# Optimization experiments

Hardware: AMD Instinct MI355X
Metric: run time of the kernel (lower is better)

## Reference

```python
import jax, jax.numpy as jnp
import numpy as np

DIM = 1024
HEADS = 16
DIM_HEAD = DIM // HEADS
SCALE = DIM_HEAD ** -0.5
LN_EPS = 1e-5


def setup_inputs() -> dict:
    key = jax.random.key(0)
    ks = jax.random.split(key, 7)
    b, n = 4, 2048
    x = jax.random.normal(ks[0], (b, n, DIM), dtype=jnp.float32)
    pos = jax.random.normal(ks[1], (b, n, DIM), dtype=jnp.float32)
    # params (torch Linear init-like scale)
    w_qkv = jax.random.normal(ks[2], (DIM, 3 * DIM), dtype=jnp.float32) * (DIM ** -0.5)
    w_out = jax.random.normal(ks[3], (DIM, DIM), dtype=jnp.float32) * (DIM ** -0.5)
    b_out = jax.random.normal(ks[4], (DIM,), dtype=jnp.float32) * 0.01
    ln_gamma = jnp.ones((DIM,), dtype=jnp.float32)
    ln_beta = jnp.zeros((DIM,), dtype=jnp.float32)
    return {"x": x, "pos": pos, "w_qkv": w_qkv, "w_out": w_out,
            "b_out": b_out, "ln_gamma": ln_gamma, "ln_beta": ln_beta}


def _layer_norm(x, gamma, beta):
    mu = jnp.mean(x, axis=-1, keepdims=True)
    var = jnp.mean(jnp.square(x - mu), axis=-1, keepdims=True)
    return (x - mu) * jax.lax.rsqrt(var + LN_EPS) * gamma + beta


def reference(x, pos, w_qkv, w_out, b_out, ln_gamma, ln_beta):
    b, n, _ = x.shape
    xn = _layer_norm(x, ln_gamma, ln_beta)
    qkv = xn @ w_qkv                                    # [b, n, 3*dim]
    q, k, v = jnp.split(qkv, 3, axis=-1)
    # [b, n, dim] -> [b, h, n, d]
    to_heads = lambda t: t.reshape(b, n, HEADS, DIM_HEAD).transpose(0, 2, 1, 3)
    q, k, v = to_heads(q), to_heads(k), to_heads(v)
    scores = jnp.einsum('bhid,bhjd->bhij', q, k) * SCALE  # [b, h, n, n]
    attn = jax.nn.softmax(scores, axis=-1)
    out = jnp.einsum('bhij,bhjd->bhid', attn, v)          # [b, h, n, d]
    out = out.transpose(0, 2, 1, 3).reshape(b, n, DIM)    # [b, n, dim]
    return (out + pos) @ w_out + b_out
```

## Files before the change

### kernel.cpp

```cpp
#include <hip/hip_runtime.h>
#include <math.h>
#include <stdint.h>

#define TOKENS 8192
#define DIM 1024
#define N3 3072
#define NSEQ 2048
#define NH 16
#define DH 64

typedef __attribute__((ext_vector_type(8))) __bf16 bf16x8;
typedef __attribute__((ext_vector_type(4))) float f32x4;
typedef __attribute__((ext_vector_type(16))) float f32x16;
typedef __attribute__((ext_vector_type(4))) short short4v;

__device__ __forceinline__ unsigned cvt2bf(float a, float b) {
    unsigned r;
    asm("v_cvt_pk_bf16_f32 %0, %1, %2" : "=v"(r) : "v"(a), "v"(b));
    return r;
}
__device__ __forceinline__ unsigned short f2bf(float f) {
    unsigned r;
    asm("v_cvt_pk_bf16_f32 %0, %1, %1" : "=v"(r) : "v"(f));
    return (unsigned short)r;
}
__device__ __forceinline__ float exp2_raw(float x) {
    float r;
    asm("v_exp_f32 %0, %1" : "=v"(r) : "v"(x));
    return r;
}
__device__ __forceinline__ float max3f(float a, float b, float c) {
    float d;
    asm("v_max3_f32 %0, %1, %2, %3" : "=v"(d) : "v"(a), "v"(b), "v"(c));
    return d;
}

__device__ __forceinline__ void glds16(const void* g, void* l) {
    __builtin_amdgcn_global_load_lds((__attribute__((address_space(1))) void*)(void*)g,
                                     (__attribute__((address_space(3))) void*)l, 16, 0, 0);
}

__global__ __launch_bounds__(256) void transpose_to_bf16(
    const float* __restrict__ in, unsigned short* __restrict__ out, int R, int C) {
    __shared__ float tile[64][65];
    int n0 = blockIdx.x * 64, k0 = blockIdx.y * 64;
    int t = threadIdx.x;
#pragma unroll
    for (int i = 0; i < 16; i++) {
        int idx = i * 256 + t;
        int r = idx >> 6, c = idx & 63;
        tile[r][c] = in[(size_t)(k0 + r) * C + n0 + c];
    }
    __syncthreads();
#pragma unroll
    for (int i = 0; i < 16; i++) {
        int idx = i * 256 + t;
        int r = idx >> 6, c = idx & 63;
        out[(size_t)(n0 + r) * R + k0 + c] = f2bf(tile[c][r]);
    }
}

__global__ __launch_bounds__(256) void ln_kernel(
    const float* __restrict__ x, const float* __restrict__ gamma,
    const float* __restrict__ beta, unsigned short* __restrict__ xn) {
    int row = blockIdx.x;
    int t = threadIdx.x;
    const float4 v = ((const float4*)(x + (size_t)row * DIM))[t];
    float s = v.x + v.y + v.z + v.w;
    float sq = v.x * v.x + v.y * v.y + v.z * v.z + v.w * v.w;
#pragma unroll
    for (int m = 1; m < 64; m <<= 1) {
        s += __shfl_xor(s, m);
        sq += __shfl_xor(sq, m);
    }
    __shared__ float ws[4], wq[4];
    int w = t >> 6, lane = t & 63;
    if (lane == 0) { ws[w] = s; wq[w] = sq; }
    __syncthreads();
    s = ws[0] + ws[1] + ws[2] + ws[3];
    sq = wq[0] + wq[1] + wq[2] + wq[3];
    float mu = s * (1.0f / DIM);
    float var = sq * (1.0f / DIM) - mu * mu;
    float rstd = rsqrtf(var + 1e-5f);
    const float4 g = ((const float4*)gamma)[t];
    const float4 bb = ((const float4*)beta)[t];
    uint2 o;
    o.x = cvt2bf((v.x - mu) * rstd * g.x + bb.x, (v.y - mu) * rstd * g.y + bb.y);
    o.y = cvt2bf((v.z - mu) * rstd * g.z + bb.z, (v.w - mu) * rstd * g.w + bb.w);
    *(uint2*)(xn + (size_t)row * DIM + t * 4) = o;
}

__device__ __forceinline__ void xcd_swizzle(int& bx, int& by) {
    int nwgx = gridDim.x;
    int nwg = nwgx * gridDim.y;
    int wg = by * nwgx + bx;
    int cpx = nwg >> 3;
    int swz = (wg & 7) * cpx + (wg >> 3);
    bx = swz % nwgx;
    by = swz / nwgx;
}

__device__ __forceinline__ void gemm_core(
    const unsigned short* __restrict__ A, const unsigned short* __restrict__ Bt, int K,
    int brow, int bcol, short* As, short* Bs, f32x4 acc[4][4]) {
    int t = threadIdx.x, w = t >> 6, lane = t & 63;
    int wr = w >> 1, wc = w & 1;
    int srow = lane >> 2, scol = (lane & 3) * 8;
    for (int k0 = 0; k0 < K; k0 += 32) {
        __syncthreads();
#pragma unroll
        for (int i = 0; i < 2; i++) {
            int c = i * 4 + w;
            glds16(A + (size_t)(brow + 16 * c + srow) * K + k0 + scol, (char*)As + c * 1024);
            glds16(Bt + (size_t)(bcol + 16 * c + srow) * K + k0 + scol, (char*)Bs + c * 1024);
        }
        __syncthreads();
        bf16x8 a[4], b[4];
#pragma unroll
        for (int i = 0; i < 4; i++) {
            a[i] = *(const bf16x8*)&As[(wr * 64 + i * 16 + (lane & 15)) * 32 + (lane >> 4) * 8];
            b[i] = *(const bf16x8*)&Bs[(wc * 64 + i * 16 + (lane & 15)) * 32 + (lane >> 4) * 8];
        }
#pragma unroll
        for (int i = 0; i < 4; i++)
#pragma unroll
            for (int j = 0; j < 4; j++)
                acc[i][j] = __builtin_amdgcn_mfma_f32_16x16x32_bf16(a[i], b[j], acc[i][j], 0, 0, 0);
    }
}

#define QSCALE_LOG2E 0.18033688011112042f

__global__ __launch_bounds__(256) void gemm_qkv(
    const unsigned short* __restrict__ A, const unsigned short* __restrict__ Bt,
    unsigned short* __restrict__ Qb, unsigned short* __restrict__ Kb,
    unsigned short* __restrict__ Vt) {
    __shared__ __align__(16) short As[128 * 32];
    __shared__ __align__(16) short Bs[128 * 32];
    int bx = blockIdx.x, by = blockIdx.y;
    xcd_swizzle(bx, by);
    int brow = by * 128, bcol = bx * 128;
    f32x4 acc[4][4] = {};
    gemm_core(A, Bt, DIM, brow, bcol, As, Bs, acc);

    int t = threadIdx.x, w = t >> 6, lane = t & 63;
    int wr = w >> 1, wc = w & 1;
    int part = bcol >> 10;
#pragma unroll
    for (int i = 0; i < 4; i++) {
#pragma unroll
        for (int j = 0; j < 4; j++) {
            int col = bcol + wc * 64 + j * 16 + (lane & 15);
            int within = col & 1023;
            int h = within >> 6, d = within & 63;
            int rowb = brow + wr * 64 + i * 16 + (lane >> 4) * 4;
            if (part == 2) {
                int b = rowb >> 11, n = rowb & 2047;
                int bh = (b << 4) + h;
                uint2 pv;
                pv.x = cvt2bf(acc[i][j][0], acc[i][j][1]);
                pv.y = cvt2bf(acc[i][j][2], acc[i][j][3]);
                *(uint2*)(Vt + ((size_t)bh * 64 + d) * 2048 + n) = pv;
            } else {
#pragma unroll
                for (int r = 0; r < 4; r++) {
                    int row = rowb + r;
                    int b = row >> 11, n = row & 2047;
                    int bh = (b << 4) + h;
                    float val = acc[i][j][r];
                    if (part == 0)
                        Qb[((size_t)bh * 2048 + n) * 64 + d] = f2bf(val * QSCALE_LOG2E);
                    else
                        Kb[((size_t)bh * 2048 + n) * 64 + d] = f2bf(val);
                }
            }
        }
    }
}

__global__ __launch_bounds__(256) void gemm_out(
    const unsigned short* __restrict__ A, const unsigned short* __restrict__ Bt,
    const float* __restrict__ bias, float* __restrict__ out) {
    __shared__ __align__(16) short As[128 * 32];
    __shared__ __align__(16) short Bs[128 * 32];
    int bx = blockIdx.x, by = blockIdx.y;
    xcd_swizzle(bx, by);
    int brow = by * 128, bcol = bx * 128;
    f32x4 acc[4][4] = {};
    gemm_core(A, Bt, DIM, brow, bcol, As, Bs, acc);

    int t = threadIdx.x, w = t >> 6, lane = t & 63;
    int wr = w >> 1, wc = w & 1;
#pragma unroll
    for (int i = 0; i < 4; i++) {
#pragma unroll
        for (int j = 0; j < 4; j++) {
            int col = bcol + wc * 64 + j * 16 + (lane & 15);
            float bv = bias[col];
#pragma unroll
            for (int r = 0; r < 4; r++) {
                int row = brow + wr * 64 + i * 16 + (lane >> 4) * 4 + r;
                out[(size_t)row * DIM + col] = acc[i][j][r] + bv;
            }
        }
    }
}

#define LOG2E_THR 11.5f

__global__ __launch_bounds__(512, 4) void attn_kernel(
    const unsigned short* __restrict__ Qb, const unsigned short* __restrict__ Kb,
    const unsigned short* __restrict__ Vt, const float* __restrict__ pos,
    unsigned short* __restrict__ att) {
    __shared__ __align__(16) char Ks[4][8192];
    __shared__ __align__(16) char Vs[4][8192];
    int t = threadIdx.x, w = t >> 6, lane = t & 63;
    int l31 = lane & 31, lhi = lane >> 5;

    int L = blockIdx.y * gridDim.x + blockIdx.x;
    int bh = (L & 7) + (((L >> 3) & 7) << 3);
    int qt = L >> 6;
    int b = bh >> 4, h = bh & 15;
    int qr = qt * 256 + w * 32 + l31;

    const unsigned short* Qh = Qb + (size_t)bh * NSEQ * DH;
    const char* Khc = (const char*)(Kb + (size_t)bh * NSEQ * DH);
    const char* Vhc = (const char*)(Vt + (size_t)bh * DH * NSEQ);

    bf16x8 qf[4];
#pragma unroll
    for (int ks = 0; ks < 4; ks++)
        qf[ks] = *(const bf16x8*)(Qh + (size_t)qr * DH + ks * 16 + lhi * 8);

    f32x16 oacc[2] = {};
    float mrun = -INFINITY, lsum = 0.f;

    int ct = w >> 2, cs = w & 3;
    const char* Ksrc = Khc + (size_t)(ct * 32 + l31) * 128 + cs * 32 + lhi * 16;
    const char* Vsrc = Vhc + (size_t)(ct * 32 + l31) * 4096 + (size_t)(cs * 16 + lhi * 8) * 2;
    auto stage = [&](char* kbuf, char* vbuf, int kv0) {
        glds16(Ksrc + (size_t)kv0 * 128, kbuf + w * 1024);
        glds16(Vsrc + (size_t)kv0 * 2, vbuf + w * 1024);
    };

    auto compute = [&](const char* kc, const char* vc) {
        f32x16 st0 = {}, st1 = {};
        __builtin_amdgcn_s_setprio(1);
#pragma unroll
        for (int ks = 0; ks < 4; ks++) {
            bf16x8 kf = *(const bf16x8*)(kc + ks * 1024 + lane * 16);
            st0 = __builtin_amdgcn_mfma_f32_32x32x16_bf16(kf, qf[ks], st0, 0, 0, 0);
        }
#pragma unroll
        for (int ks = 0; ks < 4; ks++) {
            bf16x8 kf = *(const bf16x8*)(kc + (4 + ks) * 1024 + lane * 16);
            st1 = __builtin_amdgcn_mfma_f32_32x32x16_bf16(kf, qf[ks], st1, 0, 0, 0);
        }
        __builtin_amdgcn_s_setprio(0);

        float b0 = max3f(st0[0], st0[8], st1[0]);
        float b1 = max3f(st0[1], st0[9], st1[1]);
        float b2 = max3f(st0[2], st0[10], st1[2]);
        float b3 = max3f(st0[3], st0[11], st1[3]);
        float b4 = max3f(st0[4], st0[12], st1[4]);
        float b5 = max3f(st0[5], st0[13], st1[5]);
        float b6 = max3f(st0[6], st0[14], st1[6]);
        float b7 = max3f(st0[7], st0[15], st1[7]);
        float c0 = max3f(b0, b4, st1[8]);
        float c1 = max3f(b1, b5, st1[9]);
        float c2 = max3f(b2, b6, st1[10]);
        float c3 = max3f(b3, b7, st1[11]);
        float d0 = max3f(c0, c1, st1[12]);
        float d1 = max3f(c2, c3, st1[13]);
        float pm = max3f(d0, d1, fmaxf(st1[14], st1[15]));
        {
            float pa = pm, pb = pm;
            asm("v_permlane32_swap_b32 %0, %1" : "+v"(pa), "+v"(pb));
            pm = fmaxf(pa, pb);
        }
        if (!__all(pm - mrun <= LOG2E_THR)) {
            float mnew = fmaxf(mrun, pm);
            float scale = exp2_raw(mrun - mnew);
            lsum *= scale;
            oacc[0] *= scale;
            oacc[1] *= scale;
            mrun = mnew;
        }
        {
            float s0 = 0.f, s1 = 0.f, s2 = 0.f, s3 = 0.f;
#pragma unroll
            for (int r = 0; r < 16; r += 4) {
                float e0 = exp2_raw(st0[r] - mrun);
                float e1 = exp2_raw(st0[r + 1] - mrun);
                float e2 = exp2_raw(st0[r + 2] - mrun);
                float e3 = exp2_raw(st0[r + 3] - mrun);
                st0[r] = e0; st0[r + 1] = e1; st0[r + 2] = e2; st0[r + 3] = e3;
                s0 += e0; s1 += e1; s2 += e2; s3 += e3;
            }
#pragma unroll
            for (int r = 0; r < 16; r += 4) {
                float e0 = exp2_raw(st1[r] - mrun);
                float e1 = exp2_raw(st1[r + 1] - mrun);
                float e2 = exp2_raw(st1[r + 2] - mrun);
                float e3 = exp2_raw(st1[r + 3] - mrun);
                st1[r] = e0; st1[r + 1] = e1; st1[r + 2] = e2; st1[r + 3] = e3;
                s0 += e0; s1 += e1; s2 += e2; s3 += e3;
            }
            lsum += (s0 + s1) + (s2 + s3);
        }
        bf16x8 bfr[4];
#pragma unroll
        for (int ks = 0; ks < 4; ks++) {
            const f32x16& sv = (ks < 2) ? st0 : st1;
            int rb = (ks & 1) * 8;
            unsigned pa = cvt2bf(sv[rb + 0], sv[rb + 1]);
            unsigned pc = cvt2bf(sv[rb + 2], sv[rb + 3]);
            unsigned pb = cvt2bf(sv[rb + 4], sv[rb + 5]);
            unsigned pd = cvt2bf(sv[rb + 6], sv[rb + 7]);
            asm("v_permlane32_swap_b32 %0, %1" : "+v"(pa), "+v"(pb));
            asm("v_permlane32_swap_b32 %0, %1" : "+v"(pc), "+v"(pd));
            uint4 pw = {pa, pc, pb, pd};
            bfr[ks] = *(bf16x8*)&pw;
        }
        __builtin_amdgcn_s_setprio(1);
#pragma unroll
        for (int ks = 0; ks < 4; ks++)
#pragma unroll
            for (int dt = 0; dt < 2; dt++) {
                bf16x8 vf = *(const bf16x8*)(vc + (dt * 4 + ks) * 1024 + lane * 16);
                oacc[dt] = __builtin_amdgcn_mfma_f32_32x32x16_bf16(vf, bfr[ks], oacc[dt], 0, 0, 0);
            }
        __builtin_amdgcn_s_setprio(0);
    };

    char* kA0 = Ks[0]; char* kA1 = Ks[1]; char* kB0 = Ks[2]; char* kB1 = Ks[3];
    char* vA0 = Vs[0]; char* vA1 = Vs[1]; char* vB0 = Vs[2]; char* vB1 = Vs[3];
    stage(kA0, vA0, 0);
    stage(kA1, vA1, 64);

    for (int p = 0; p < 32; p += 2) {
        asm volatile("s_waitcnt vmcnt(2)" ::: "memory");
        __builtin_amdgcn_s_barrier();
        stage(kB0, vB0, ((p + 2) & 31) << 6);
        stage(kB1, vB1, ((p + 3) & 31) << 6);
        compute(kA0, vA0);
        asm volatile("s_waitcnt vmcnt(4)" ::: "memory");
        compute(kA1, vA1);
        char* tp;
        tp = kA0; kA0 = kB0; kB0 = tp;  tp = kA1; kA1 = kB1; kB1 = tp;
        tp = vA0; vA0 = vB0; vB0 = tp;  tp = vA1; vA1 = vB1; vB1 = tp;
    }

    {
        float pa = lsum, pb = lsum;
        asm("v_permlane32_swap_b32 %0, %1" : "+v"(pa), "+v"(pb));
        lsum = pa + pb;
    }
    float inv = 1.0f / lsum;
    size_t rowbase = ((size_t)b * NSEQ + qr) * DIM + h * 64;
#pragma unroll
    for (int dt = 0; dt < 2; dt++)
#pragma unroll
        for (int g4 = 0; g4 < 4; g4++) {
            int d = dt * 32 + g4 * 8 + lhi * 4;
            float4 pv = *(const float4*)(pos + rowbase + d);
            uint2 o;
            o.x = cvt2bf(oacc[dt][g4 * 4 + 0] * inv + pv.x, oacc[dt][g4 * 4 + 1] * inv + pv.y);
            o.y = cvt2bf(oacc[dt][g4 * 4 + 2] * inv + pv.z, oacc[dt][g4 * 4 + 3] * inv + pv.w);
            *(uint2*)(att + rowbase + d) = o;
        }
}

extern "C" void kernel_launch(void* const* d_in, const int* in_sizes, int n_in,
                              void* d_out, int out_size, void* d_ws, size_t ws_size,
                              hipStream_t stream) {
    const float* x = (const float*)d_in[0];
    const float* pos = (const float*)d_in[1];
    const float* w_qkv = (const float*)d_in[2];
    const float* w_out = (const float*)d_in[3];
    const float* b_out = (const float*)d_in[4];
    const float* ln_g = (const float*)d_in[5];
    const float* ln_b = (const float*)d_in[6];
    float* out = (float*)d_out;

    char* ws = (char*)d_ws;
    unsigned short* xn      = (unsigned short*)(ws);
    unsigned short* wqkv_bt = (unsigned short*)(ws + (16ull << 20));
    unsigned short* wout_bt = (unsigned short*)(ws + (22ull << 20));
    unsigned short* Qb      = (unsigned short*)(ws + (24ull << 20));
    unsigned short* Kb      = (unsigned short*)(ws + (40ull << 20));
    unsigned short* Vt      = (unsigned short*)(ws + (56ull << 20));
    unsigned short* att     = xn;

    transpose_to_bf16<<<dim3(N3 / 64, DIM / 64), 256, 0, stream>>>(w_qkv, wqkv_bt, DIM, N3);
    transpose_to_bf16<<<dim3(DIM / 64, DIM / 64), 256, 0, stream>>>(w_out, wout_bt, DIM, DIM);
    ln_kernel<<<TOKENS, 256, 0, stream>>>(x, ln_g, ln_b, xn);
    gemm_qkv<<<dim3(N3 / 128, TOKENS / 128), 256, 0, stream>>>(xn, wqkv_bt, Qb, Kb, Vt);
    attn_kernel<<<dim3(NSEQ / 256, 64), 512, 0, stream>>>(Qb, Kb, Vt, pos, att);
    gemm_out<<<dim3(DIM / 128, TOKENS / 128), 256, 0, stream>>>(att, wout_bt, b_out, out);
}
```

Baseline: 218.4 us.

## Triple-buffer GEMM shared-memory tiles with async prefetch two stages ahead

Replaces the load-sync-compute GEMM loop with a three-stage LDS ring buffer. Global-to-LDS loads run two k-tiles ahead, and a vmcnt wait plus one barrier per iteration replaces the two syncthreads. MFMA issue is wrapped in raised wave priority. The goal is to hide global load latency behind matrix math in both projection GEMMs. In exchange, LDS use per block triples, which can lower occupancy. The wraparound prefetch in the last iterations also issues redundant loads.

```diff
diff --git a/kernel.cpp b/kernel.cpp
--- a/kernel.cpp
+++ b/kernel.cpp
@@ -100,32 +100,49 @@
     by = swz / nwgx;
 }
 
+__device__ __forceinline__ void gemm_stage(
+    const unsigned short* __restrict__ A, const unsigned short* __restrict__ Bt, int K,
+    int brow, int bcol, int k0, char* Abuf, char* Bbuf, int w, int srow, int scol) {
+#pragma unroll
+    for (int i = 0; i < 2; i++) {
+        int c = i * 4 + w;
+        glds16(A + (size_t)(brow + 16 * c + srow) * K + k0 + scol, Abuf + c * 1024);
+        glds16(Bt + (size_t)(bcol + 16 * c + srow) * K + k0 + scol, Bbuf + c * 1024);
+    }
+}
+
 __device__ __forceinline__ void gemm_core(
     const unsigned short* __restrict__ A, const unsigned short* __restrict__ Bt, int K,
-    int brow, int bcol, short* As, short* Bs, f32x4 acc[4][4]) {
+    int brow, int bcol, char* As, char* Bs, f32x4 acc[4][4]) {
     int t = threadIdx.x, w = t >> 6, lane = t & 63;
     int wr = w >> 1, wc = w & 1;
     int srow = lane >> 2, scol = (lane & 3) * 8;
-    for (int k0 = 0; k0 < K; k0 += 32) {
-        __syncthreads();
-#pragma unroll
-        for (int i = 0; i < 2; i++) {
-            int c = i * 4 + w;
-            glds16(A + (size_t)(brow + 16 * c + srow) * K + k0 + scol, (char*)As + c * 1024);
-            glds16(Bt + (size_t)(bcol + 16 * c + srow) * K + k0 + scol, (char*)Bs + c * 1024);
-        }
-        __syncthreads();
+    char* a0 = As; char* a1 = As + 8192; char* a2 = As + 16384;
+    char* b0 = Bs; char* b1 = Bs + 8192; char* b2 = Bs + 16384;
+    gemm_stage(A, Bt, K, brow, bcol, 0, a0, b0, w, srow, scol);
+    gemm_stage(A, Bt, K, brow, bcol, 32, a1, b1, w, srow, scol);
+    int NT = K >> 5;
+    for (int kt = 0; kt < NT; kt++) {
+        asm volatile("s_waitcnt vmcnt(4)" ::: "memory");
+        __builtin_amdgcn_s_barrier();
+        int kn = kt + 2; if (kn >= NT) kn -= NT;
+        gemm_stage(A, Bt, K, brow, bcol, kn << 5, a2, b2, w, srow, scol);
         bf16x8 a[4], b[4];
 #pragma unroll
         for (int i = 0; i < 4; i++) {
-            a[i] = *(const bf16x8*)&As[(wr * 64 + i * 16 + (lane & 15)) * 32 + (lane >> 4) * 8];
-            b[i] = *(const bf16x8*)&Bs[(wc * 64 + i * 16 + (lane & 15)) * 32 + (lane >> 4) * 8];
-        }
+            a[i] = *(const bf16x8*)(a0 + (wr * 64 + i * 16 + (lane & 15)) * 64 + (lane >> 4) * 16);
+            b[i] = *(const bf16x8*)(b0 + (wc * 64 + i * 16 + (lane & 15)) * 64 + (lane >> 4) * 16);
+        }
+        __builtin_amdgcn_s_setprio(1);
 #pragma unroll
         for (int i = 0; i < 4; i++)
 #pragma unroll
             for (int j = 0; j < 4; j++)
                 acc[i][j] = __builtin_amdgcn_mfma_f32_16x16x32_bf16(a[i], b[j], acc[i][j], 0, 0, 0);
+        __builtin_amdgcn_s_setprio(0);
+        char* tp;
+        tp = a0; a0 = a1; a1 = a2; a2 = tp;
+        tp = b0; b0 = b1; b1 = b2; b2 = tp;
     }
 }
 
@@ -135,8 +152,8 @@
     const unsigned short* __restrict__ A, const unsigned short* __restrict__ Bt,
     unsigned short* __restrict__ Qb, unsigned short* __restrict__ Kb,
     unsigned short* __restrict__ Vt) {
-    __shared__ __align__(16) short As[128 * 32];
-    __shared__ __align__(16) short Bs[128 * 32];
+    __shared__ __align__(16) char As[3 * 8192];
+    __shared__ __align__(16) char Bs[3 * 8192];
     int bx = blockIdx.x, by = blockIdx.y;
     xcd_swizzle(bx, by);
     int brow = by * 128, bcol = bx * 128;
@@ -181,8 +198,8 @@
 __global__ __launch_bounds__(256) void gemm_out(
     const unsigned short* __restrict__ A, const unsigned short* __restrict__ Bt,
     const float* __restrict__ bias, float* __restrict__ out) {
-    __shared__ __align__(16) short As[128 * 32];
-    __shared__ __align__(16) short Bs[128 * 32];
+    __shared__ __align__(16) char As[3 * 8192];
+    __shared__ __align__(16) char Bs[3 * 8192];
     int bx = blockIdx.x, by = blockIdx.y;
     xcd_swizzle(bx, by);
     int brow = by * 128, bcol = bx * 128;
```

Measured after the change: 216.9 us. Within noise of the previous version (-0.7%).
